# Kernel tuning notes

Hardware: AMD Instinct MI355X
Metric: run time of the kernel (lower is better)

## Reference

```python
import jax, jax.numpy as jnp
import numpy as np

B = 4096          # number of bags (sequences)
L_AVG = 2048      # average bag length
T = B * L_AVG     # total instances
P = 1 << 20       # param count for L1 penalty
ALPHA = 1e-3
BETA = 0.1
MIN_STD = 1.0
MAX_STD = 1000.0


def setup_inputs() -> dict:
    key = jax.random.key(0)
    k1, k2, k3, k4 = jax.random.split(key, 4)
    # ragged lengths with fixed total T (pairwise perturbation keeps the sum exact)
    rng = np.random.default_rng(0)
    d = rng.integers(-1024, 1025, size=B // 2)
    lengths_np = np.full(B, L_AVG, dtype=np.int64)
    lengths_np[: B // 2] += d
    lengths_np[B // 2 :] -= d
    assert lengths_np.sum() == T and lengths_np.min() >= 1
    seg_ids_np = np.repeat(np.arange(B, dtype=np.int64), lengths_np)
    return {
        "logits": jax.random.normal(k1, (B, 2), dtype=jnp.float32),
        "params": jax.random.normal(k2, (P,), dtype=jnp.float32),
        "attn_weights": jax.random.uniform(k3, (T,), dtype=jnp.float32),
        "labels": jax.random.randint(k4, (B,), 0, 2, dtype=jnp.int64),
        "lengths": jnp.asarray(lengths_np),
        "seg_ids": jnp.asarray(seg_ids_np),
    }


def reference(logits, params, attn_weights, labels, lengths, seg_ids):
    dt = attn_weights.dtype
    n = attn_weights.shape[0]
    seg = lambda v: jax.ops.segment_sum(v, seg_ids, num_segments=B)

    # CrossEntropyLoss (mean reduction)
    logp = jax.nn.log_softmax(logits, axis=-1)
    nll = -jnp.mean(jnp.take_along_axis(logp, labels[:, None], axis=1))

    lengths_f = lengths.astype(dt)
    # position within segment -> x = (pos+1)/len, per-segment arange(1..L)/L
    starts = jnp.cumsum(lengths) - lengths
    pos = jnp.arange(n) - starts[seg_ids]
    x = (pos + 1).astype(dt) / lengths_f[seg_ids]

    y = attn_weights
    sum_y = seg(y)                         # [B]
    mean = seg(x * y) / sum_y              # [B] per-seg attention mean
    ideal_std = jnp.where(labels == 1, MIN_STD, MAX_STD).astype(dt) / lengths_f
    z = (x - mean[seg_ids]) / ideal_std[seg_ids]
    inv_norm = 1.0 / (ideal_std[seg_ids] * jnp.sqrt(2.0 * jnp.pi).astype(dt))
    r_hat = jnp.exp(-0.5 * z * z) * inv_norm
    r = r_hat / (seg(r_hat)[seg_ids] + 1e-6)
    r = jax.lax.stop_gradient(r)           # torch computes r under no_grad

    penalty = (ALPHA / 2) * jnp.sum(jnp.abs(params))
    diff = y - r
    attn_penalty = (BETA / 2) * jnp.mean(seg(diff * diff) / lengths_f)
    loss = nll + penalty + attn_penalty
    return loss, nll
```

## Files before the change

kernel.cpp:

```cpp
#include <hip/hip_runtime.h>


constexpr float INV_SQRT_2PI = 0.39894228040143267794f;
constexpr float NEG_HALF_LOG2E = -0.72134752044448170368f;
constexpr int L1_BLOCKS = 512;


__global__ __launch_bounds__(256) void main_kernel(
    const float* __restrict__ logits, const float* __restrict__ params,
    const float* __restrict__ attn, const int* __restrict__ labels,
    const int* __restrict__ lengths, int P, int Bn, int segBlocks,
    float* __restrict__ segpart, float* __restrict__ l1part,
    float* __restrict__ nllpart) {
  const int tid = threadIdx.x, lane = tid & 63, wv = tid >> 6;
  const int bid = blockIdx.x;

  if (bid < segBlocks) {
    int wid = (bid << 2) + wv;
    if (wid >= Bn) return;

    int sacc = 0;
    const int4* l4 = (const int4*)lengths;
    int nq = wid >> 2;
    for (int q = lane; q < nq; q += 64) {
      int4 v = l4[q];
      sacc += (v.x + v.y) + (v.z + v.w);
    }
    if (lane < (wid & 3)) sacc += lengths[(wid & ~3) + lane];
#pragma unroll
    for (int off = 32; off; off >>= 1) sacc += __shfl_xor(sacc, off, 64);
    int start = sacc;
    int L = lengths[wid];
    int lab = labels[wid];

    const float* a = attn + start;
    float invL = 1.0f / (float)L;
    int head = (4 - (start & 3)) & 3;
    if (head > L) head = L;
    int nb = (L - head) >> 2;
    int tail = L - head - (nb << 2);
    const float4* a4 = (const float4*)(a + head);

    float sy = 0.f, sxy = 0.f, syy = 0.f;
    auto momA = [&](const float4& v, int q) {
      float x0 = (float)(head + (q << 2) + 1) * invL;
      sy += (v.x + v.y) + (v.z + v.w);
      sxy = fmaf(x0, v.x, fmaf(x0 + invL, v.y,
            fmaf(x0 + 2.f * invL, v.z, fmaf(x0 + 3.f * invL, v.w, sxy))));
      syy = fmaf(v.x, v.x, fmaf(v.y, v.y, fmaf(v.z, v.z, fmaf(v.w, v.w, syy))));
    };
    if (lane < head) {
      float y = a[lane];
      float x = (float)(lane + 1) * invL;
      sy += y; sxy = fmaf(x, y, sxy); syy = fmaf(y, y, syy);
    }
    if (lane < tail) {
      int i = head + (nb << 2) + lane;
      float y = a[i];
      float x = (float)(i + 1) * invL;
      sy += y; sxy = fmaf(x, y, sxy); syy = fmaf(y, y, syy);
    }
    for (int q = lane; q < nb; q += 256) {
      int q1 = q + 64, q2 = q + 128, q3 = q + 192;
      bool g1 = q1 < nb, g2 = q2 < nb, g3 = q3 < nb;
      float4 v0 = a4[q];
      float4 v1, v2, v3;
      if (g1) v1 = a4[q1];
      if (g2) v2 = a4[q2];
      if (g3) v3 = a4[q3];
      momA(v0, q);
      if (g1) momA(v1, q1);
      if (g2) momA(v2, q2);
      if (g3) momA(v3, q3);
    }
#pragma unroll
    for (int off = 32; off; off >>= 1) {
      sy  += __shfl_xor(sy, off, 64);
      sxy += __shfl_xor(sxy, off, 64);
    }
    float mean = sxy / sy;
    float inv_std = (lab == 1) ? (float)L : (float)L * 0.001f;
    float dz = invL * inv_std;

    float se = 0.f, sye = 0.f, see = 0.f;
    auto momB = [&](const float4& v, int q) {
      float z0 = ((float)(head + (q << 2) + 1) * invL - mean) * inv_std;
      float z1 = z0 + dz, z2 = z1 + dz, z3 = z2 + dz;
      float e0 = exp2f(z0 * z0 * NEG_HALF_LOG2E);
      float e1 = exp2f(z1 * z1 * NEG_HALF_LOG2E);
      float e2 = exp2f(z2 * z2 * NEG_HALF_LOG2E);
      float e3 = exp2f(z3 * z3 * NEG_HALF_LOG2E);
      se += (e0 + e1) + (e2 + e3);
      sye = fmaf(v.x, e0, fmaf(v.y, e1, fmaf(v.z, e2, fmaf(v.w, e3, sye))));
      see = fmaf(e0, e0, fmaf(e1, e1, fmaf(e2, e2, fmaf(e3, e3, see))));
    };
    if (lane < head) {
      float y = a[lane];
      float z = ((float)(lane + 1) * invL - mean) * inv_std;
      float e = exp2f(z * z * NEG_HALF_LOG2E);
      se += e; sye = fmaf(y, e, sye); see = fmaf(e, e, see);
    }
    if (lane < tail) {
      int i = head + (nb << 2) + lane;
      float y = a[i];
      float z = ((float)(i + 1) * invL - mean) * inv_std;
      float e = exp2f(z * z * NEG_HALF_LOG2E);
      se += e; sye = fmaf(y, e, sye); see = fmaf(e, e, see);
    }
    for (int q = lane; q < nb; q += 256) {
      int q1 = q + 64, q2 = q + 128, q3 = q + 192;
      bool g1 = q1 < nb, g2 = q2 < nb, g3 = q3 < nb;
      float4 v0 = a4[q];
      float4 v1, v2, v3;
      if (g1) v1 = a4[q1];
      if (g2) v2 = a4[q2];
      if (g3) v3 = a4[q3];
      momB(v0, q);
      if (g1) momB(v1, q1);
      if (g2) momB(v2, q2);
      if (g3) momB(v3, q3);
    }
#pragma unroll
    for (int off = 32; off; off >>= 1) {
      syy += __shfl_xor(syy, off, 64);
      se  += __shfl_xor(se, off, 64);
      sye += __shfl_xor(sye, off, 64);
      see += __shfl_xor(see, off, 64);
    }
    if (lane == 0) {
      float inv_norm = INV_SQRT_2PI * inv_std;
      float den = fmaf(inv_norm, se, 1e-6f);
      float inv_den = 1.0f / den;
      float c = inv_norm * inv_den;
      float d2 = syy - 2.0f * sye * c + see * (c * c);
      segpart[wid] = d2 * invL;
    }
  } else if (bid < segBlocks + L1_BLOCKS) {
    int b = bid - segBlocks;
    const float4* p4 = (const float4*)params;
    int n4 = P >> 2;
    float s = 0.f;
    for (int i = (b << 8) + tid; i < n4; i += (L1_BLOCKS << 8)) {
      float4 v = p4[i];
      s += (fabsf(v.x) + fabsf(v.y)) + (fabsf(v.z) + fabsf(v.w));
    }
    if (b == 0) {
      for (int i = (n4 << 2) + tid; i < P; i += 256) s += fabsf(params[i]);
    }
#pragma unroll
    for (int off = 32; off; off >>= 1) s += __shfl_xor(s, off, 64);
    if (lane == 0) l1part[(b << 2) + wv] = s;
  } else {
    const float2* lg2 = (const float2*)logits;
    float s = 0.f;
    for (int r = tid; r < Bn; r += 256) {
      float2 lg = lg2[r];
      float m = fmaxf(lg.x, lg.y);
      float lse = m + logf(expf(lg.x - m) + expf(lg.y - m));
      s += lse - ((labels[r] == 1) ? lg.y : lg.x);
    }
#pragma unroll
    for (int off = 32; off; off >>= 1) s += __shfl_xor(s, off, 64);
    if (lane == 0) nllpart[wv] = s;
  }
}

__global__ __launch_bounds__(256) void final_kernel(
    const float* __restrict__ segpart, const float* __restrict__ l1part,
    const float* __restrict__ nllpart, float* __restrict__ out, int Bn) {
  __shared__ double sA[4], sB[4], sC[4];
  int tid = threadIdx.x, lane = tid & 63, wv = tid >> 6;
  double accS = 0.0, accL = 0.0, accN = 0.0;
  const float4* s4 = (const float4*)segpart;
  for (int i = tid; i < (Bn >> 2); i += 256) {
    float4 v = s4[i];
    accS += ((double)v.x + (double)v.y) + ((double)v.z + (double)v.w);
  }
  for (int i = (Bn & ~3) + tid; i < Bn; i += 256) accS += (double)segpart[i];
  const float4* l4 = (const float4*)l1part;
  for (int i = tid; i < L1_BLOCKS; i += 256) {
    float4 v = l4[i];
    accL += ((double)v.x + (double)v.y) + ((double)v.z + (double)v.w);
  }
  if (tid < 4) accN = (double)nllpart[tid];
#pragma unroll
  for (int off = 32; off; off >>= 1) {
    accS += __shfl_down(accS, off, 64);
    accL += __shfl_down(accL, off, 64);
    accN += __shfl_down(accN, off, 64);
  }
  if (lane == 0) { sA[wv] = accS; sB[wv] = accL; sC[wv] = accN; }
  __syncthreads();
  if (tid == 0) {
    double segsum = (sA[0] + sA[1]) + (sA[2] + sA[3]);
    double l1     = (sB[0] + sB[1]) + (sB[2] + sB[3]);
    double nllsum = (sC[0] + sC[1]) + (sC[2] + sC[3]);
    double nll = nllsum / (double)Bn;
    double loss = nll + 5e-4 * l1 + 0.05 * (segsum / (double)Bn);
    out[0] = (float)loss;
    out[1] = (float)nll;
  }
}

extern "C" void kernel_launch(void* const* d_in, const int* in_sizes, int n_in,
                              void* d_out, int out_size, void* d_ws, size_t ws_size,
                              hipStream_t stream) {
  const float* logits  = (const float*)d_in[0];
  const float* params  = (const float*)d_in[1];
  const float* attn    = (const float*)d_in[2];
  const int*   labels  = (const int*)d_in[3];
  const int*   lengths = (const int*)d_in[4];

  int Bn = in_sizes[3];
  int P  = in_sizes[1];
  int segBlocks = (Bn + 3) / 4;

  float* segpart = (float*)d_ws;
  float* l1part  = (float*)((char*)d_ws + 16384);
  float* nllpart = (float*)((char*)d_ws + 24576);

  int grid = segBlocks + L1_BLOCKS + 1;
  hipLaunchKernelGGL(main_kernel, dim3(grid), dim3(256), 0, stream,
                     logits, params, attn, labels, lengths, P, Bn, segBlocks,
                     segpart, l1part, nllpart);
  hipLaunchKernelGGL(final_kernel, dim3(1), dim3(256), 0, stream,
                     segpart, l1part, nllpart, (float*)d_out, Bn);
}
```

Before: 114.9 us.

## Split each segment across two wavefronts and combine partial moments in LDS

Each bag is now processed by two wavefronts instead of one. Each wave strides over half the float4 chunks, and the partial sums are merged through shared memory with block barriers between the mean pass and the Gaussian pass. The sum of squares of y moves into the second pass so the first pass carries fewer accumulators. The L1 block count is halved. This doubles the number of in-flight waves working on the latency-bound segment passes, at the cost of two __syncthreads per block and some redundant prefix-sum work per wave.

```diff
diff --git a/kernel.cpp b/kernel.cpp
--- a/kernel.cpp
+++ b/kernel.cpp
@@ -3,7 +3,7 @@
 
 constexpr float INV_SQRT_2PI = 0.39894228040143267794f;
 constexpr float NEG_HALF_LOG2E = -0.72134752044448170368f;
-constexpr int L1_BLOCKS = 512;
+constexpr int L1_BLOCKS = 256;
 
 
 __global__ __launch_bounds__(256) void main_kernel(
@@ -16,8 +16,13 @@
   const int bid = blockIdx.x;
 
   if (bid < segBlocks) {
-    int wid = (bid << 2) + wv;
-    if (wid >= Bn) return;
+    __shared__ float sA2[2][2][2];
+    __shared__ float sB2[2][2][4];
+    int si = wv >> 1;
+    int h  = wv & 1;
+    int wid0 = (bid << 1) + si;
+    bool valid = wid0 < Bn;
+    int wid = valid ? wid0 : (Bn - 1);
 
     int sacc = 0;
     const int4* l4 = (const int4*)lengths;
@@ -41,27 +46,26 @@
     int tail = L - head - (nb << 2);
     const float4* a4 = (const float4*)(a + head);
 
-    float sy = 0.f, sxy = 0.f, syy = 0.f;
+    float sy = 0.f, sxy = 0.f;
     auto momA = [&](const float4& v, int q) {
       float x0 = (float)(head + (q << 2) + 1) * invL;
       sy += (v.x + v.y) + (v.z + v.w);
       sxy = fmaf(x0, v.x, fmaf(x0 + invL, v.y,
             fmaf(x0 + 2.f * invL, v.z, fmaf(x0 + 3.f * invL, v.w, sxy))));
-      syy = fmaf(v.x, v.x, fmaf(v.y, v.y, fmaf(v.z, v.z, fmaf(v.w, v.w, syy))));
     };
-    if (lane < head) {
+    if (h == 0 && lane < head) {
       float y = a[lane];
       float x = (float)(lane + 1) * invL;
-      sy += y; sxy = fmaf(x, y, sxy); syy = fmaf(y, y, syy);
-    }
-    if (lane < tail) {
+      sy += y; sxy = fmaf(x, y, sxy);
+    }
+    if (h == 1 && lane < tail) {
       int i = head + (nb << 2) + lane;
       float y = a[i];
       float x = (float)(i + 1) * invL;
-      sy += y; sxy = fmaf(x, y, sxy); syy = fmaf(y, y, syy);
-    }
-    for (int q = lane; q < nb; q += 256) {
-      int q1 = q + 64, q2 = q + 128, q3 = q + 192;
+      sy += y; sxy = fmaf(x, y, sxy);
+    }
+    for (int q = lane + (h << 6); q < nb; q += 512) {
+      int q1 = q + 128, q2 = q + 256, q3 = q + 384;
       bool g1 = q1 < nb, g2 = q2 < nb, g3 = q3 < nb;
       float4 v0 = a4[q];
       float4 v1, v2, v3;
@@ -78,11 +82,15 @@
       sy  += __shfl_xor(sy, off, 64);
       sxy += __shfl_xor(sxy, off, 64);
     }
-    float mean = sxy / sy;
+    if (lane == 0) { sA2[si][h][0] = sy; sA2[si][h][1] = sxy; }
+    __syncthreads();
+    float toty  = sA2[si][0][0] + sA2[si][1][0];
+    float totxy = sA2[si][0][1] + sA2[si][1][1];
+    float mean = totxy / toty;
     float inv_std = (lab == 1) ? (float)L : (float)L * 0.001f;
     float dz = invL * inv_std;
 
-    float se = 0.f, sye = 0.f, see = 0.f;
+    float syy = 0.f, se = 0.f, sye = 0.f, see = 0.f;
     auto momB = [&](const float4& v, int q) {
       float z0 = ((float)(head + (q << 2) + 1) * invL - mean) * inv_std;
       float z1 = z0 + dz, z2 = z1 + dz, z3 = z2 + dz;
@@ -90,25 +98,28 @@
       float e1 = exp2f(z1 * z1 * NEG_HALF_LOG2E);
       float e2 = exp2f(z2 * z2 * NEG_HALF_LOG2E);
       float e3 = exp2f(z3 * z3 * NEG_HALF_LOG2E);
+      syy = fmaf(v.x, v.x, fmaf(v.y, v.y, fmaf(v.z, v.z, fmaf(v.w, v.w, syy))));
       se += (e0 + e1) + (e2 + e3);
       sye = fmaf(v.x, e0, fmaf(v.y, e1, fmaf(v.z, e2, fmaf(v.w, e3, sye))));
       see = fmaf(e0, e0, fmaf(e1, e1, fmaf(e2, e2, fmaf(e3, e3, see))));
     };
-    if (lane < head) {
+    if (h == 0 && lane < head) {
       float y = a[lane];
       float z = ((float)(lane + 1) * invL - mean) * inv_std;
       float e = exp2f(z * z * NEG_HALF_LOG2E);
+      syy = fmaf(y, y, syy);
       se += e; sye = fmaf(y, e, sye); see = fmaf(e, e, see);
     }
-    if (lane < tail) {
+    if (h == 1 && lane < tail) {
       int i = head + (nb << 2) + lane;
       float y = a[i];
       float z = ((float)(i + 1) * invL - mean) * inv_std;
       float e = exp2f(z * z * NEG_HALF_LOG2E);
+      syy = fmaf(y, y, syy);
       se += e; sye = fmaf(y, e, sye); see = fmaf(e, e, see);
     }
-    for (int q = lane; q < nb; q += 256) {
-      int q1 = q + 64, q2 = q + 128, q3 = q + 192;
+    for (int q = lane + (h << 6); q < nb; q += 512) {
+      int q1 = q + 128, q2 = q + 256, q3 = q + 384;
       bool g1 = q1 < nb, g2 = q2 < nb, g3 = q3 < nb;
       float4 v0 = a4[q];
       float4 v1, v2, v3;
@@ -128,11 +139,19 @@
       see += __shfl_xor(see, off, 64);
     }
     if (lane == 0) {
+      sB2[si][h][0] = syy; sB2[si][h][1] = se;
+      sB2[si][h][2] = sye; sB2[si][h][3] = see;
+    }
+    __syncthreads();
+    if (valid && h == 0 && lane == 0) {
+      float tyy = sB2[si][0][0] + sB2[si][1][0];
+      float tse = sB2[si][0][1] + sB2[si][1][1];
+      float tye = sB2[si][0][2] + sB2[si][1][2];
+      float tee = sB2[si][0][3] + sB2[si][1][3];
       float inv_norm = INV_SQRT_2PI * inv_std;
-      float den = fmaf(inv_norm, se, 1e-6f);
-      float inv_den = 1.0f / den;
-      float c = inv_norm * inv_den;
-      float d2 = syy - 2.0f * sye * c + see * (c * c);
+      float den = fmaf(inv_norm, tse, 1e-6f);
+      float c = inv_norm / den;
+      float d2 = tyy - 2.0f * tye * c + tee * (c * c);
       segpart[wid] = d2 * invL;
     }
   } else if (bid < segBlocks + L1_BLOCKS) {
@@ -213,7 +232,7 @@
 
   int Bn = in_sizes[3];
   int P  = in_sizes[1];
-  int segBlocks = (Bn + 3) / 4;
+  int segBlocks = (Bn + 1) / 2;
 
   float* segpart = (float*)d_ws;
   float* l1part  = (float*)((char*)d_ws + 16384);
```

Result: no change. 115.8 us (+0.7%).
